# Optimization experiments

Measured on AMD Instinct MI355X. Metric: run time of the kernel, lower is better.

The kernel has to match this reference:

```python
import jax, jax.numpy as jnp
import numpy as np

N_IN, N_HID, N_OUT = 128, 1024, 64
B, T = 128, 256
SIGMA_NEU = 0.05
ALPHA = 0.25

def setup_inputs() -> dict:
    key = jax.random.key(0)
    ks = jax.random.split(key, 6)
    input_signal = jax.random.normal(ks[0], (B, T, N_IN), dtype=jnp.float32)
    hidden = jax.random.normal(ks[1], (B, N_HID), dtype=jnp.float32)
    w_in_w = jax.random.normal(ks[2], (N_HID, N_IN), dtype=jnp.float32) / np.sqrt(N_IN)
    w_hh_w = jax.random.normal(ks[3], (N_HID, N_HID), dtype=jnp.float32) / np.sqrt(N_HID)
    w_hh_b = jnp.zeros((N_HID,), dtype=jnp.float32)
    w_out_w = jax.random.normal(ks[4], (N_OUT, N_HID), dtype=jnp.float32) / np.sqrt(N_HID)
    alpha = jnp.full((N_HID,), ALPHA, dtype=jnp.float32)
    noise_raw = jax.random.normal(ks[5], (B, N_HID), dtype=jnp.float32)
    return {
        'input_signal': input_signal,
        'hidden': hidden,
        'w_in_w': w_in_w,
        'w_hh_w': w_hh_w,
        'w_hh_b': w_hh_b,
        'w_out_w': w_out_w,
        'alpha': alpha,
        'noise_raw': noise_raw,
        'perturbation_timing': 100,
    }

def reference(input_signal, hidden, w_in_w, w_hh_w, w_hh_b, w_out_w, alpha, noise_raw, perturbation_timing):
    # input_signal: [B, T, n_in] -> time-major [T, B, n_in]
    x = jnp.swapaxes(input_signal, 0, 1)
    length = x.shape[0]
    # neural noise injected only at t == perturbation_timing (torch: randn*sigma*sqrt(alpha))
    noise = noise_raw * SIGMA_NEU * jnp.sqrt(alpha)

    def step(h, inp):
        t, x_t = inp
        activated = jnp.tanh(h)
        tmp = x_t @ w_in_w.T + activated @ w_hh_w.T + w_hh_b  # [B, n_hid]
        h_new = (1.0 - alpha) * h + alpha * tmp
        h_new = jnp.where(t == perturbation_timing, h_new + noise, h_new)
        out = h_new @ w_out_w.T  # [B, n_out]
        return h_new, (h_new, out)

    h_final, (hs, outs) = jax.lax.scan(step, hidden, (jnp.arange(length), x))
    hidden_list = jnp.swapaxes(hs, 0, 1)   # [B, T, n_hid]
    output_list = jnp.swapaxes(outs, 0, 1)  # [B, T, n_out]
    return hidden_list, output_list, h_final
```

## Files before the change

### kernel.cpp

```cpp
#include <hip/hip_runtime.h>

typedef _Float16 half8 __attribute__((ext_vector_type(8)));
typedef float floatx4 __attribute__((ext_vector_type(4)));
typedef float floatx2 __attribute__((ext_vector_type(2)));

#define N_IN   128
#define N_HID  1024
#define N_OUT  64
#define BB     128
#define TT     256

#define WHH_STRIDE 1032
#define WIN_STRIDE 136
#define RED_STRIDE 33

__device__ __forceinline__ float tanh_fast(float v) {
    float e = __expf(2.0f * v);
    return 1.0f - 2.0f / (e + 1.0f);
}

__global__ __launch_bounds__(256, 1) void rnn_seq_kernel(
    const float* __restrict__ x,
    const float* __restrict__ h0,
    const float* __restrict__ w_in,
    const float* __restrict__ w_hh,
    const float* __restrict__ w_hh_b,
    const float* __restrict__ alpha,
    const float* __restrict__ noise_raw,
    const int* __restrict__ pt_ptr,
    float* __restrict__ out,
    _Float16* __restrict__ actbuf,
    unsigned int* __restrict__ flags)
{
    __shared__ _Float16 Whh_hi[32 * WHH_STRIDE];
    __shared__ _Float16 Whh_lo[32 * WHH_STRIDE];
    __shared__ _Float16 Win_hi[32 * WIN_STRIDE];
    __shared__ _Float16 Win_lo[32 * WIN_STRIDE];
    __shared__ float red[4 * 16 * RED_STRIDE];

    const int tid  = threadIdx.x;
    const int bid  = blockIdx.x;
    const int g    = bid & 7;
    const int s    = bid >> 3;
    const int w    = tid >> 6;
    const int lane = tid & 63;
    const int quad = lane >> 4;
    const int mrow = lane & 15;

    for (int p = 0; p < 32; ++p) {
        int f4 = tid + (p << 8);
        int c  = f4 >> 8;
        int k4 = (f4 & 255) << 2;
        floatx4 wv = *(const floatx4*)(w_hh + ((size_t)(s * 32 + c) << 10) + k4);
        #pragma unroll
        for (int i = 0; i < 4; ++i) {
            float v = wv[i];
            _Float16 hi = (_Float16)v;
            _Float16 lo = (_Float16)((v - (float)hi) * 1024.0f);
            Whh_hi[c * WHH_STRIDE + k4 + i] = hi;
            Whh_lo[c * WHH_STRIDE + k4 + i] = lo;
        }
    }
    for (int p = 0; p < 4; ++p) {
        int f4 = tid + (p << 8);
        int c  = f4 >> 5;
        int k4 = (f4 & 31) << 2;
        floatx4 wv = *(const floatx4*)(w_in + ((size_t)(s * 32 + c) << 7) + k4);
        #pragma unroll
        for (int i = 0; i < 4; ++i) {
            float v = wv[i];
            _Float16 hi = (_Float16)v;
            _Float16 lo = (_Float16)((v - (float)hi) * 1024.0f);
            Win_hi[c * WIN_STRIDE + k4 + i] = hi;
            Win_lo[c * WIN_STRIDE + k4 + i] = lo;
        }
    }
    __syncthreads();

    half8 bh0[8], bl0[8], bh1[8], bl1[8];
    #pragma unroll
    for (int kc = 0; kc < 8; ++kc) {
        int kb = (w << 8) + (kc << 5) + (quad << 3);
        bh0[kc] = *(const half8*)&Whh_hi[mrow * WHH_STRIDE + kb];
        bl0[kc] = *(const half8*)&Whh_lo[mrow * WHH_STRIDE + kb];
        bh1[kc] = *(const half8*)&Whh_hi[(16 + mrow) * WHH_STRIDE + kb];
        bl1[kc] = *(const half8*)&Whh_lo[(16 + mrow) * WHH_STRIDE + kb];
    }
    half8 wi_h0, wi_l0, wi_h1, wi_l1;
    {
        int kb = (w << 5) + (quad << 3);
        wi_h0 = *(const half8*)&Win_hi[mrow * WIN_STRIDE + kb];
        wi_l0 = *(const half8*)&Win_lo[mrow * WIN_STRIDE + kb];
        wi_h1 = *(const half8*)&Win_hi[(16 + mrow) * WIN_STRIDE + kb];
        wi_l1 = *(const half8*)&Win_lo[(16 + mrow) * WIN_STRIDE + kb];
    }

    const int r   = tid >> 4;
    const int c2  = tid & 15;
    const int b   = g * 16 + r;
    const int j0  = s * 32 + 2 * c2;
    const floatx2 a2  = *(const floatx2*)&alpha[j0];
    const floatx2 bi2 = *(const floatx2*)&w_hh_b[j0];
    const floatx2 nr2 = *(const floatx2*)&noise_raw[((size_t)b << 10) + j0];
    const float n0 = nr2.x * 0.05f * __builtin_sqrtf(a2.x);
    const float n1 = nr2.y * 0.05f * __builtin_sqrtf(a2.y);
    const int pt = *pt_ptr;
    floatx2 h2 = *(const floatx2*)&h0[((size_t)b << 10) + j0];
    float hA = h2.x, hB = h2.y;

    {
        unsigned int* act1_32 = (unsigned int*)(actbuf + BB * N_HID);
        union { _Float16 h[2]; unsigned int u; } pk;
        pk.h[0] = (_Float16)tanh_fast(hA);
        pk.h[1] = (_Float16)tanh_fast(hB);
        __hip_atomic_store(&act1_32[(((unsigned)b << 10) + j0) >> 1], pk.u,
                           __ATOMIC_RELAXED, __HIP_MEMORY_SCOPE_AGENT);
    }
    __syncthreads();
    if (tid == 0)
        __hip_atomic_store(&flags[((unsigned)g) * 32u + s], 1u,
                           __ATOMIC_RELAXED, __HIP_MEMORY_SCOPE_AGENT);

    float* hidden_list = out;
    float* h_final = out + (size_t)BB * TT * N_HID + (size_t)BB * TT * N_OUT;
    const int arow = g * 16 + mrow;

    for (int t = 0; t < TT; ++t) {
        {
            const unsigned tok = (unsigned)t + 1u;
            const unsigned fidx = ((unsigned)t * 8u + g) * 32u + (w << 3) + (lane & 7);
            while (true) {
                unsigned v = __hip_atomic_load(&flags[fidx], __ATOMIC_RELAXED,
                                               __HIP_MEMORY_SCOPE_AGENT);
                if (__ballot(v == tok) == ~0ull) break;
                __builtin_amdgcn_s_sleep(1);
            }
        }

        half8 afr[8];
        {
            const unsigned long long* actq = (const unsigned long long*)
                (actbuf + (size_t)((t & 1) ^ 1) * (BB * N_HID));
            const unsigned long long* p =
                actq + ((((size_t)arow << 10) + (w << 8) + (quad << 3)) >> 2);
            #pragma unroll
            for (int kc = 0; kc < 8; ++kc) {
                union { unsigned long long u[2]; half8 h; } cv;
                cv.u[0] = __hip_atomic_load(p + kc * 8,     __ATOMIC_RELAXED,
                                            __HIP_MEMORY_SCOPE_AGENT);
                cv.u[1] = __hip_atomic_load(p + kc * 8 + 1, __ATOMIC_RELAXED,
                                            __HIP_MEMORY_SCOPE_AGENT);
                afr[kc] = cv.h;
            }
        }
        half8 xfr;
        {
            const float* xp = x + (((size_t)arow << 8) + t) * N_IN + (w << 5) + (quad << 3);
            floatx4 x0 = *(const floatx4*)xp;
            floatx4 x1 = *(const floatx4*)(xp + 4);
            #pragma unroll
            for (int i = 0; i < 4; ++i) { xfr[i] = (_Float16)x0[i]; xfr[4 + i] = (_Float16)x1[i]; }
        }

        floatx4 acch0 = {0.f,0.f,0.f,0.f}, acch1 = {0.f,0.f,0.f,0.f};
        floatx4 accl0 = {0.f,0.f,0.f,0.f}, accl1 = {0.f,0.f,0.f,0.f};

        acch0 = __builtin_amdgcn_mfma_f32_16x16x32_f16(xfr, wi_h0, acch0, 0, 0, 0);
        accl0 = __builtin_amdgcn_mfma_f32_16x16x32_f16(xfr, wi_l0, accl0, 0, 0, 0);
        acch1 = __builtin_amdgcn_mfma_f32_16x16x32_f16(xfr, wi_h1, acch1, 0, 0, 0);
        accl1 = __builtin_amdgcn_mfma_f32_16x16x32_f16(xfr, wi_l1, accl1, 0, 0, 0);

        #pragma unroll
        for (int kc = 0; kc < 8; ++kc) {
            acch0 = __builtin_amdgcn_mfma_f32_16x16x32_f16(afr[kc], bh0[kc], acch0, 0, 0, 0);
            accl0 = __builtin_amdgcn_mfma_f32_16x16x32_f16(afr[kc], bl0[kc], accl0, 0, 0, 0);
            acch1 = __builtin_amdgcn_mfma_f32_16x16x32_f16(afr[kc], bh1[kc], acch1, 0, 0, 0);
            accl1 = __builtin_amdgcn_mfma_f32_16x16x32_f16(afr[kc], bl1[kc], accl1, 0, 0, 0);
        }

        #pragma unroll
        for (int rr = 0; rr < 4; ++rr) {
            red[(w * 16 + quad * 4 + rr) * RED_STRIDE + mrow]
                = acch0[rr] + accl0[rr] * (1.0f / 1024.0f);
            red[(w * 16 + quad * 4 + rr) * RED_STRIDE + 16 + mrow]
                = acch1[rr] + accl1[rr] * (1.0f / 1024.0f);
        }
        __syncthreads();

        float t0v = bi2.x, t1v = bi2.y;
        #pragma unroll
        for (int ww = 0; ww < 4; ++ww) {
            t0v += red[(ww * 16 + r) * RED_STRIDE + 2 * c2];
            t1v += red[(ww * 16 + r) * RED_STRIDE + 2 * c2 + 1];
        }
        hA = (1.0f - a2.x) * hA + a2.x * t0v;
        hB = (1.0f - a2.y) * hB + a2.y * t1v;
        if (t == pt) { hA += n0; hB += n1; }

        floatx2 hv = {hA, hB};
        *(floatx2*)&hidden_list[(((size_t)b << 8) + t) * N_HID + j0] = hv;

        {
            union { _Float16 h[2]; unsigned int u; } pk;
            pk.h[0] = (_Float16)tanh_fast(hA);
            pk.h[1] = (_Float16)tanh_fast(hB);
            unsigned int* actw32 = (unsigned int*)(actbuf + (size_t)(t & 1) * (BB * N_HID));
            __hip_atomic_store(&actw32[(((unsigned)b << 10) + j0) >> 1], pk.u,
                               __ATOMIC_RELAXED, __HIP_MEMORY_SCOPE_AGENT);
        }

        __syncthreads();
        if (tid == 0)
            __hip_atomic_store(&flags[((unsigned)(t + 1) * 8u + g) * 32u + s],
                               (unsigned)t + 2u,
                               __ATOMIC_RELAXED, __HIP_MEMORY_SCOPE_AGENT);
    }

    *(floatx2*)&h_final[((size_t)b << 10) + j0] = (floatx2){hA, hB};
}

__global__ __launch_bounds__(256) void out_gemm_kernel(
    const float* __restrict__ hl,
    const float* __restrict__ w_out,
    float* __restrict__ outp)
{
    __shared__ _Float16 Wb[64 * 264];
    const int tid  = threadIdx.x;
    const int w    = tid >> 6;
    const int lane = tid & 63;
    const int quad = lane >> 4;
    const int mrow = lane & 15;
    const size_t rowbase = (size_t)blockIdx.x << 6;

    floatx4 acc0 = {0.f,0.f,0.f,0.f}, acc1 = {0.f,0.f,0.f,0.f};
    floatx4 acc2 = {0.f,0.f,0.f,0.f}, acc3 = {0.f,0.f,0.f,0.f};

    for (int kc = 0; kc < 4; ++kc) {
        __syncthreads();
        for (int p = 0; p < 16; ++p) {
            int f4 = tid + (p << 8);
            int n  = f4 >> 6;
            int k4 = (f4 & 63) << 2;
            floatx4 wv = *(const floatx4*)(w_out + ((size_t)n << 10) + (kc << 8) + k4);
            #pragma unroll
            for (int i = 0; i < 4; ++i) Wb[n * 264 + k4 + i] = (_Float16)wv[i];
        }
        __syncthreads();
        for (int kk = 0; kk < 8; ++kk) {
            const float* ap = hl + (rowbase + (w << 4) + mrow) * 1024
                                 + (kc << 8) + (kk << 5) + (quad << 3);
            floatx4 a0v = *(const floatx4*)ap;
            floatx4 a1v = *(const floatx4*)(ap + 4);
            half8 afr;
            #pragma unroll
            for (int i = 0; i < 4; ++i) { afr[i] = (_Float16)a0v[i]; afr[4 + i] = (_Float16)a1v[i]; }
            int kb = (kk << 5) + (quad << 3);
            half8 bf0 = *(const half8*)&Wb[(mrow)      * 264 + kb];
            half8 bf1 = *(const half8*)&Wb[(16 + mrow) * 264 + kb];
            half8 bf2 = *(const half8*)&Wb[(32 + mrow) * 264 + kb];
            half8 bf3 = *(const half8*)&Wb[(48 + mrow) * 264 + kb];
            acc0 = __builtin_amdgcn_mfma_f32_16x16x32_f16(afr, bf0, acc0, 0, 0, 0);
            acc1 = __builtin_amdgcn_mfma_f32_16x16x32_f16(afr, bf1, acc1, 0, 0, 0);
            acc2 = __builtin_amdgcn_mfma_f32_16x16x32_f16(afr, bf2, acc2, 0, 0, 0);
            acc3 = __builtin_amdgcn_mfma_f32_16x16x32_f16(afr, bf3, acc3, 0, 0, 0);
        }
    }
    size_t rb = rowbase + (w << 4);
    #pragma unroll
    for (int rr = 0; rr < 4; ++rr) {
        outp[(rb + quad * 4 + rr) * 64 +      mrow] = acc0[rr];
        outp[(rb + quad * 4 + rr) * 64 + 16 + mrow] = acc1[rr];
        outp[(rb + quad * 4 + rr) * 64 + 32 + mrow] = acc2[rr];
        outp[(rb + quad * 4 + rr) * 64 + 48 + mrow] = acc3[rr];
    }
}

extern "C" void kernel_launch(void* const* d_in, const int* in_sizes, int n_in,
                              void* d_out, int out_size, void* d_ws, size_t ws_size,
                              hipStream_t stream)
{
    const float* x      = (const float*)d_in[0];
    const float* h0     = (const float*)d_in[1];
    const float* w_in   = (const float*)d_in[2];
    const float* w_hh   = (const float*)d_in[3];
    const float* w_hh_b = (const float*)d_in[4];
    const float* w_out  = (const float*)d_in[5];
    const float* alpha  = (const float*)d_in[6];
    const float* noise  = (const float*)d_in[7];
    const int*   pt     = (const int*)d_in[8];
    float* out = (float*)d_out;

    _Float16* actbuf = (_Float16*)d_ws;
    unsigned int* flags =
        (unsigned int*)((char*)d_ws + (size_t)2 * BB * N_HID * sizeof(_Float16));

    hipLaunchKernelGGL(rnn_seq_kernel, dim3(256), dim3(256), 0, stream,
                       x, h0, w_in, w_hh, w_hh_b, alpha, noise, pt, out, actbuf, flags);

    float* output_list = out + (size_t)BB * TT * N_HID;
    hipLaunchKernelGGL(out_gemm_kernel, dim3(512), dim3(256), 0, stream,
                       out, w_out, output_list);
}
```

Baseline: 1.202 ms.

## Use per-wave flags and double-buffered reduction to remove block barrier per step

Each wave now publishes its own readiness flag after a vmcnt wait, instead of a block-wide barrier followed by a single thread's store. Consumers poll 32 per-wave flags per group, and the reduction buffer is double-buffered so the trailing barrier can go. The x load is issued before the spin-wait and the hidden_list store is moved after the flag publish, which takes both off the critical path. Whh staging is split into two halves to cut shared memory. In exchange the flag array is four times larger, polling traffic grows, and correctness relies on vmcnt ordering rather than release semantics.

```diff
diff --git a/kernel.cpp b/kernel.cpp
--- a/kernel.cpp
+++ b/kernel.cpp
@@ -32,11 +32,11 @@
     _Float16* __restrict__ actbuf,
     unsigned int* __restrict__ flags)
 {
-    __shared__ _Float16 Whh_hi[32 * WHH_STRIDE];
-    __shared__ _Float16 Whh_lo[32 * WHH_STRIDE];
+    __shared__ _Float16 Whh_hi[16 * WHH_STRIDE];
+    __shared__ _Float16 Whh_lo[16 * WHH_STRIDE];
     __shared__ _Float16 Win_hi[32 * WIN_STRIDE];
     __shared__ _Float16 Win_lo[32 * WIN_STRIDE];
-    __shared__ float red[4 * 16 * RED_STRIDE];
+    __shared__ float red[2][64 * RED_STRIDE];
 
     const int tid  = threadIdx.x;
     const int bid  = blockIdx.x;
@@ -47,7 +47,9 @@
     const int quad = lane >> 4;
     const int mrow = lane & 15;
 
-    for (int p = 0; p < 32; ++p) {
+    half8 bh0[8], bl0[8], bh1[8], bl1[8];
+
+    for (int p = 0; p < 16; ++p) {
         int f4 = tid + (p << 8);
         int c  = f4 >> 8;
         int k4 = (f4 & 255) << 2;
@@ -61,6 +63,28 @@
             Whh_lo[c * WHH_STRIDE + k4 + i] = lo;
         }
     }
+    __syncthreads();
+    #pragma unroll
+    for (int kc = 0; kc < 8; ++kc) {
+        int kb = (w << 8) + (kc << 5) + (quad << 3);
+        bh0[kc] = *(const half8*)&Whh_hi[mrow * WHH_STRIDE + kb];
+        bl0[kc] = *(const half8*)&Whh_lo[mrow * WHH_STRIDE + kb];
+    }
+    __syncthreads();
+    for (int p = 0; p < 16; ++p) {
+        int f4 = tid + (p << 8);
+        int c  = f4 >> 8;
+        int k4 = (f4 & 255) << 2;
+        floatx4 wv = *(const floatx4*)(w_hh + ((size_t)(s * 32 + 16 + c) << 10) + k4);
+        #pragma unroll
+        for (int i = 0; i < 4; ++i) {
+            float v = wv[i];
+            _Float16 hi = (_Float16)v;
+            _Float16 lo = (_Float16)((v - (float)hi) * 1024.0f);
+            Whh_hi[c * WHH_STRIDE + k4 + i] = hi;
+            Whh_lo[c * WHH_STRIDE + k4 + i] = lo;
+        }
+    }
     for (int p = 0; p < 4; ++p) {
         int f4 = tid + (p << 8);
         int c  = f4 >> 5;
@@ -76,15 +100,11 @@
         }
     }
     __syncthreads();
-
-    half8 bh0[8], bl0[8], bh1[8], bl1[8];
     #pragma unroll
     for (int kc = 0; kc < 8; ++kc) {
         int kb = (w << 8) + (kc << 5) + (quad << 3);
-        bh0[kc] = *(const half8*)&Whh_hi[mrow * WHH_STRIDE + kb];
-        bl0[kc] = *(const half8*)&Whh_lo[mrow * WHH_STRIDE + kb];
-        bh1[kc] = *(const half8*)&Whh_hi[(16 + mrow) * WHH_STRIDE + kb];
-        bl1[kc] = *(const half8*)&Whh_lo[(16 + mrow) * WHH_STRIDE + kb];
+        bh1[kc] = *(const half8*)&Whh_hi[mrow * WHH_STRIDE + kb];
+        bl1[kc] = *(const half8*)&Whh_lo[mrow * WHH_STRIDE + kb];
     }
     half8 wi_h0, wi_l0, wi_h1, wi_l1;
     {
@@ -108,6 +128,8 @@
     floatx2 h2 = *(const floatx2*)&h0[((size_t)b << 10) + j0];
     float hA = h2.x, hB = h2.y;
 
+    const unsigned pslot = ((unsigned)(s >> 3)) * 32u + ((unsigned)(s & 7)) * 4u + w;
+
     {
         unsigned int* act1_32 = (unsigned int*)(actbuf + BB * N_HID);
         union { _Float16 h[2]; unsigned int u; } pk;
@@ -116,9 +138,9 @@
         __hip_atomic_store(&act1_32[(((unsigned)b << 10) + j0) >> 1], pk.u,
                            __ATOMIC_RELAXED, __HIP_MEMORY_SCOPE_AGENT);
     }
-    __syncthreads();
-    if (tid == 0)
-        __hip_atomic_store(&flags[((unsigned)g) * 32u + s], 1u,
+    asm volatile("s_waitcnt vmcnt(0)" ::: "memory");
+    if (lane == 0)
+        __hip_atomic_store(&flags[((unsigned)g << 7) + pslot], 1u,
                            __ATOMIC_RELAXED, __HIP_MEMORY_SCOPE_AGENT);
 
     float* hidden_list = out;
@@ -126,11 +148,16 @@
     const int arow = g * 16 + mrow;
 
     for (int t = 0; t < TT; ++t) {
+        const float* xp = x + (((size_t)arow << 8) + t) * N_IN + (w << 5) + (quad << 3);
+        floatx4 x0 = *(const floatx4*)xp;
+        floatx4 x1 = *(const floatx4*)(xp + 4);
+
         {
             const unsigned tok = (unsigned)t + 1u;
-            const unsigned fidx = ((unsigned)t * 8u + g) * 32u + (w << 3) + (lane & 7);
+            const unsigned int* fp =
+                flags + ((((unsigned)t << 3) + g) << 7) + ((unsigned)w << 5) + (lane & 31);
             while (true) {
-                unsigned v = __hip_atomic_load(&flags[fidx], __ATOMIC_RELAXED,
+                unsigned v = __hip_atomic_load(fp, __ATOMIC_RELAXED,
                                                __HIP_MEMORY_SCOPE_AGENT);
                 if (__ballot(v == tok) == ~0ull) break;
                 __builtin_amdgcn_s_sleep(1);
@@ -154,13 +181,8 @@
             }
         }
         half8 xfr;
-        {
-            const float* xp = x + (((size_t)arow << 8) + t) * N_IN + (w << 5) + (quad << 3);
-            floatx4 x0 = *(const floatx4*)xp;
-            floatx4 x1 = *(const floatx4*)(xp + 4);
-            #pragma unroll
-            for (int i = 0; i < 4; ++i) { xfr[i] = (_Float16)x0[i]; xfr[4 + i] = (_Float16)x1[i]; }
-        }
+        #pragma unroll
+        for (int i = 0; i < 4; ++i) { xfr[i] = (_Float16)x0[i]; xfr[4 + i] = (_Float16)x1[i]; }
 
         floatx4 acch0 = {0.f,0.f,0.f,0.f}, acch1 = {0.f,0.f,0.f,0.f};
         floatx4 accl0 = {0.f,0.f,0.f,0.f}, accl1 = {0.f,0.f,0.f,0.f};
@@ -178,11 +200,12 @@
             accl1 = __builtin_amdgcn_mfma_f32_16x16x32_f16(afr[kc], bl1[kc], accl1, 0, 0, 0);
         }
 
+        float* redp = red[t & 1];
         #pragma unroll
         for (int rr = 0; rr < 4; ++rr) {
-            red[(w * 16 + quad * 4 + rr) * RED_STRIDE + mrow]
+            redp[(w * 16 + quad * 4 + rr) * RED_STRIDE + mrow]
                 = acch0[rr] + accl0[rr] * (1.0f / 1024.0f);
-            red[(w * 16 + quad * 4 + rr) * RED_STRIDE + 16 + mrow]
+            redp[(w * 16 + quad * 4 + rr) * RED_STRIDE + 16 + mrow]
                 = acch1[rr] + accl1[rr] * (1.0f / 1024.0f);
         }
         __syncthreads();
@@ -190,15 +213,12 @@
         float t0v = bi2.x, t1v = bi2.y;
         #pragma unroll
         for (int ww = 0; ww < 4; ++ww) {
-            t0v += red[(ww * 16 + r) * RED_STRIDE + 2 * c2];
-            t1v += red[(ww * 16 + r) * RED_STRIDE + 2 * c2 + 1];
+            t0v += redp[(ww * 16 + r) * RED_STRIDE + 2 * c2];
+            t1v += redp[(ww * 16 + r) * RED_STRIDE + 2 * c2 + 1];
         }
         hA = (1.0f - a2.x) * hA + a2.x * t0v;
         hB = (1.0f - a2.y) * hB + a2.y * t1v;
         if (t == pt) { hA += n0; hB += n1; }
-
-        floatx2 hv = {hA, hB};
-        *(floatx2*)&hidden_list[(((size_t)b << 8) + t) * N_HID + j0] = hv;
 
         {
             union { _Float16 h[2]; unsigned int u; } pk;
@@ -208,12 +228,14 @@
             __hip_atomic_store(&actw32[(((unsigned)b << 10) + j0) >> 1], pk.u,
                                __ATOMIC_RELAXED, __HIP_MEMORY_SCOPE_AGENT);
         }
-
-        __syncthreads();
-        if (tid == 0)
-            __hip_atomic_store(&flags[((unsigned)(t + 1) * 8u + g) * 32u + s],
+        asm volatile("s_waitcnt vmcnt(0)" ::: "memory");
+        if (lane == 0)
+            __hip_atomic_store(&flags[((((unsigned)(t + 1) << 3) + g) << 7) + pslot],
                                (unsigned)t + 2u,
                                __ATOMIC_RELAXED, __HIP_MEMORY_SCOPE_AGENT);
+
+        floatx2 hv = {hA, hB};
+        *(floatx2*)&hidden_list[(((size_t)b << 8) + t) * N_HID + j0] = hv;
     }
 
     *(floatx2*)&h_final[((size_t)b << 10) + j0] = (floatx2){hA, hB};
```

After: 1.592 ms. 32.4% more time.
